# Optimization experiments

Measured on AMD Instinct MI355X. Metric: run time of the kernel, lower is better.

## Reference

```python
import jax, jax.numpy as jnp
import numpy as np

B, N, F, T, K, FO = 16, 1024, 64, 24, 3, 64


def setup_inputs() -> dict:
    key = jax.random.key(0)
    ks = jax.random.split(key, 8)
    sc = 0.05
    x = jax.random.normal(ks[0], (B, N, F, T), dtype=jnp.float32)
    W1 = jax.random.normal(ks[1], (T,), dtype=jnp.float32) * sc
    W2 = jax.random.normal(ks[2], (F, T), dtype=jnp.float32) * sc
    W3 = jax.random.normal(ks[3], (F,), dtype=jnp.float32) * sc
    bs = jax.random.normal(ks[4], (1, N, N), dtype=jnp.float32) * sc
    Vs = jax.random.normal(ks[5], (N, N), dtype=jnp.float32) * sc
    cheb = jax.random.normal(ks[6], (K, N, N), dtype=jnp.float32) * sc
    Theta = jax.random.normal(ks[7], (K, F, FO), dtype=jnp.float32) * sc
    return {"x": x, "W1": W1, "W2": W2, "W3": W3, "bs": bs, "Vs": Vs,
            "cheb": cheb, "Theta": Theta}


def spatial_attention(x, W1, W2, W3, bs, Vs):
    # x: (B,N,F,T) -> S: (B,N,N)
    lhs = jnp.einsum('bnft,t->bnf', x, W1)          # (B,N,F)
    lhs = jnp.einsum('bnf,ft->bnt', lhs, W2)        # (B,N,T)
    rhs = jnp.einsum('f,bnft->btn', W3, x)          # (B,T,N)
    product = jnp.einsum('bnt,btm->bnm', lhs, rhs)  # (B,N,N)
    S = jnp.einsum('ik,bkj->bij', Vs, jax.nn.sigmoid(product + bs))
    return jax.nn.softmax(S, axis=1)


def reference(x, W1, W2, W3, bs, Vs, cheb, Theta):
    # x: (B,N,F,T); cheb: (K,N,N); Theta: (K,F,FO)
    S = spatial_attention(x, W1, W2, W3, bs, Vs)    # (B,N,N)
    out = jnp.zeros((x.shape[0], x.shape[1], Theta.shape[2], x.shape[3]),
                    dtype=x.dtype)
    for k in range(cheb.shape[0]):                  # small fixed K
        Tat = cheb[k] * S                           # (B,N,N) attention-masked T_k
        # T_k_with_at.permute(0,2,1) @ graph_signal, vectorized over t
        r = jnp.einsum('bnm,bnft->bmft', Tat, x)    # (B,N,F,T)
        out = out + jnp.einsum('bmft,fo->bmot', r, Theta[k])
    return jax.nn.relu(out)                         # (B,N,FO,T)
```

## Files before the change

### kernel.cpp

```cpp
#include <hip/hip_runtime.h>
#include <math.h>

#define Bc 16
#define Nc 1024
#define Fc 64
#define Tc 24
#define Kc 3
#define FOc 64
#define Cc (Fc*Tc)
#define KKc (Kc*Nc)

typedef __attribute__((ext_vector_type(8))) short short8;
typedef __attribute__((ext_vector_type(8))) unsigned short u16x8;
typedef __attribute__((ext_vector_type(4))) float f32x4;

__device__ __forceinline__ unsigned short f2bf(float f) {
  unsigned u = __float_as_uint(f);
  u += 0x7fff + ((u >> 16) & 1);
  return (unsigned short)(u >> 16);
}
__device__ __forceinline__ float bf2f(unsigned short h) {
  return __uint_as_float((unsigned)h << 16);
}

#define GLL16(g, l) __builtin_amdgcn_global_load_lds( \
    (const __attribute__((address_space(1))) void*)(g), \
    (__attribute__((address_space(3))) void*)(l), 16, 0, 0)

__device__ __forceinline__ f32x4 mfma16(short8 a, short8 b, f32x4 c) {
  return __builtin_amdgcn_mfma_f32_16x16x32_bf16(a, b, c, 0, 0, 0);
}

__device__ __forceinline__ void gemm_core(
    const unsigned short* __restrict__ Ag, const unsigned short* __restrict__ Bg,
    int lda, int ldb, int K,
    unsigned short* As, unsigned short* Bs,
    int wave, int lane, f32x4 acc[4][4]) {
  int sr = lane >> 3;
  int sc = ((lane & 7) ^ sr) * 8;
  const unsigned short* a0 = Ag + (size_t)(wave * 32 + sr) * lda + sc;
  const unsigned short* b0 = Bg + (size_t)(wave * 32 + sr) * ldb + sc;
  unsigned short* asw = As + (wave * 32) * 64;
  unsigned short* bsw = Bs + (wave * 32) * 64;
  int rw = (wave >> 1) * 64, cw = (wave & 1) * 64;
  int frow = lane & 15;
  int q = lane >> 4;
  int p0 = (q ^ (frow & 7)) * 8;
  int p1 = ((q | 4) ^ (frow & 7)) * 8;
  for (int k0 = 0; k0 < K; k0 += 64) {
    #pragma unroll
    for (int c = 0; c < 4; ++c) {
      GLL16(a0 + (size_t)(c * 8) * lda + k0, asw + (c * 8) * 64);
      GLL16(b0 + (size_t)(c * 8) * ldb + k0, bsw + (c * 8) * 64);
    }
    __syncthreads();
    #pragma unroll
    for (int h = 0; h < 2; ++h) {
      int p = h ? p1 : p0;
      short8 afr[4], bfr[4];
      #pragma unroll
      for (int i = 0; i < 4; ++i)
        afr[i] = *(const short8*)&As[(rw + i * 16 + frow) * 64 + p];
      #pragma unroll
      for (int j = 0; j < 4; ++j)
        bfr[j] = *(const short8*)&Bs[(cw + j * 16 + frow) * 64 + p];
      #pragma unroll
      for (int i = 0; i < 4; ++i)
        #pragma unroll
        for (int j = 0; j < 4; ++j)
          acc[i][j] = mfma16(afr[i], bfr[j], acc[i][j]);
    }
    __syncthreads();
  }
}

__global__ __launch_bounds__(256) void xprep_kernel(
    const float* __restrict__ x, const float* __restrict__ W1,
    const float* __restrict__ W2, const float* __restrict__ W3,
    unsigned short* __restrict__ xt2, unsigned short* __restrict__ lhsb,
    unsigned short* __restrict__ rhsb) {
  __shared__ float ld[4 * 1560];
  __shared__ float af[4 * 64];
  int w = threadIdx.x >> 6, lane = threadIdx.x & 63;
  size_t n = (size_t)blockIdx.x * 4 + w;
  const float* xp = x + n * Cc;
  float* lw = ld + w * 1560;
  #pragma unroll
  for (int j = 0; j < 24; ++j) {
    int i = j * 64 + lane;
    int f = i / 24, t = i - f * 24;
    lw[t * 65 + f] = xp[i];
  }
  __syncthreads();
  float a = 0.f;
  #pragma unroll
  for (int t = 0; t < Tc; ++t) a += lw[t * 65 + lane] * W1[t];
  af[w * 64 + lane] = a;
  #pragma unroll
  for (int j = 0; j < 24; ++j)
    xt2[n * Cc + j * 64 + lane] = f2bf(lw[j * 65 + lane]);
  __syncthreads();
  float l = 0.f, r = 0.f;
  if (lane < Tc) {
    #pragma unroll 8
    for (int f = 0; f < Fc; ++f) {
      l += af[w * 64 + f] * W2[f * Tc + lane];
      r += W3[f] * lw[lane * 65 + f];
    }
  }
  lhsb[n * 64 + lane] = (lane < Tc) ? f2bf(l) : (unsigned short)0;
  rhsb[n * 64 + lane] = (lane < Tc) ? f2bf(r) : (unsigned short)0;
}

__global__ __launch_bounds__(256) void misc_kernel(
    const float* __restrict__ Vs, const float* __restrict__ Theta,
    const float* __restrict__ bs, unsigned short* __restrict__ Vsbf,
    unsigned short* __restrict__ tcat, float* __restrict__ bsT) {
  __shared__ float t[64 * 65];
  int bid = blockIdx.x, tid = threadIdx.x;
  if (bid < 1024) {
    int i = (bid * 256 + tid) * 4;
    float4 v = *(const float4*)&Vs[i];
    ushort4 o;
    o.x = f2bf(v.x); o.y = f2bf(v.y); o.z = f2bf(v.z); o.w = f2bf(v.w);
    *(ushort4*)&Vsbf[i] = o;
  } else if (bid < 1088) {
    int i = (bid - 1024) * 256 + tid;
    int m2 = i >> 6, f = i & 63;
    int k = m2 >> 6, o = m2 & 63;
    tcat[i] = (m2 < 192) ? f2bf(Theta[((size_t)k * Fc + f) * FOc + o])
                         : (unsigned short)0;
  } else {
    int id = bid - 1088;
    int p0 = (id >> 4) * 64, q0 = (id & 15) * 64;
    #pragma unroll
    for (int s = 0; s < 4; ++s) {
      int qr = (tid >> 4) + s * 16, pc = (tid & 15) * 4;
      float4 v = *(const float4*)&bs[(size_t)(q0 + qr) * Nc + p0 + pc];
      t[(pc + 0) * 65 + qr] = v.x;
      t[(pc + 1) * 65 + qr] = v.y;
      t[(pc + 2) * 65 + qr] = v.z;
      t[(pc + 3) * 65 + qr] = v.w;
    }
    __syncthreads();
    #pragma unroll
    for (int s = 0; s < 4; ++s) {
      int pr = (tid >> 4) + s * 16, qc = (tid & 15) * 4;
      float4 v = {t[pr * 65 + qc], t[pr * 65 + qc + 1],
                  t[pr * 65 + qc + 2], t[pr * 65 + qc + 3]};
      *(float4*)&bsT[(size_t)(p0 + pr) * Nc + q0 + qc] = v;
    }
  }
}

__global__ __launch_bounds__(256) void chebT_kernel(
    const float* __restrict__ cheb, float* __restrict__ chebT) {
  int k = blockIdx.z;
  int n0 = blockIdx.y * 64, m0 = blockIdx.x * 64;
  __shared__ float t[64 * 65];
  const float* src = cheb + (size_t)k * Nc * Nc;
  float* dst = chebT + (size_t)k * Nc * Nc;
  int tid = threadIdx.x;
  #pragma unroll
  for (int s = 0; s < 4; ++s) {
    int nr = (tid >> 4) + s * 16, mc = (tid & 15) * 4;
    float4 v = *(const float4*)&src[(size_t)(n0 + nr) * Nc + m0 + mc];
    t[(mc + 0) * 65 + nr] = v.x;
    t[(mc + 1) * 65 + nr] = v.y;
    t[(mc + 2) * 65 + nr] = v.z;
    t[(mc + 3) * 65 + nr] = v.w;
  }
  __syncthreads();
  #pragma unroll
  for (int s = 0; s < 4; ++s) {
    int mr = (tid >> 4) + s * 16, nc = (tid & 15) * 4;
    float4 v = {t[mr * 65 + nc], t[mr * 65 + nc + 1], t[mr * 65 + nc + 2], t[mr * 65 + nc + 3]};
    *(float4*)&dst[(size_t)(m0 + mr) * Nc + n0 + nc] = v;
  }
}

__global__ __launch_bounds__(256) void masksoft_kernel(
    const float* __restrict__ chebT, const unsigned short* __restrict__ ST,
    unsigned short* __restrict__ Acat, int bbase) {
  int m  = blockIdx.x & (Nc - 1);
  int bl = blockIdx.x >> 10;
  int tid = threadIdx.x;
  const unsigned short* sp = ST + ((size_t)(bbase + bl) * Nc + m) * Nc;
  ushort4 s4 = *(const ushort4*)(sp + tid * 4);
  float v0 = bf2f(s4.x), v1 = bf2f(s4.y), v2 = bf2f(s4.z), v3 = bf2f(s4.w);
  __shared__ float redm[4], reds[4];
  int wave = tid >> 6, lane = tid & 63;
  float mx = fmaxf(fmaxf(v0, v1), fmaxf(v2, v3));
  #pragma unroll
  for (int off = 32; off; off >>= 1) mx = fmaxf(mx, __shfl_xor(mx, off));
  if (lane == 0) redm[wave] = mx;
  __syncthreads();
  mx = fmaxf(fmaxf(redm[0], redm[1]), fmaxf(redm[2], redm[3]));
  float e0 = __expf(v0 - mx), e1 = __expf(v1 - mx);
  float e2 = __expf(v2 - mx), e3 = __expf(v3 - mx);
  float sm = e0 + e1 + e2 + e3;
  #pragma unroll
  for (int off = 32; off; off >>= 1) sm += __shfl_xor(sm, off);
  if (lane == 0) reds[wave] = sm;
  __syncthreads();
  float inv = 1.f / (reds[0] + reds[1] + reds[2] + reds[3]);
  e0 *= inv; e1 *= inv; e2 *= inv; e3 *= inv;
  unsigned short* ap = Acat + ((size_t)bl * Nc + m) * KKc + tid * 4;
  #pragma unroll
  for (int k = 0; k < Kc; ++k) {
    float4 c = *(const float4*)&chebT[((size_t)k * Nc + m) * Nc + tid * 4];
    ushort4 o;
    o.x = f2bf(c.x * e0); o.y = f2bf(c.y * e1);
    o.z = f2bf(c.z * e2); o.w = f2bf(c.w * e3);
    *(ushort4*)(ap + k * Nc) = o;
  }
}

template <int MODE>
__global__ __launch_bounds__(256) void mfma_gemm_bt(
    const unsigned short* __restrict__ A, const unsigned short* __restrict__ B,
    void* __restrict__ Cv, const float* __restrict__ bias, int K, int CN,
    long long Abatch, long long Bbatch, long long Cbatch) {
  __shared__ unsigned short As[128 * 64];
  __shared__ unsigned short Bs[128 * 64];
  int gx = gridDim.x, gy = gridDim.y;
  int nwg = gx * gy * gridDim.z;
  int bid = blockIdx.x + gx * (blockIdx.y + gy * blockIdx.z);
  int xcd = bid & 7, idx = bid >> 3;
  int qq = nwg >> 3, rr = nwg & 7;
  int lin = (xcd < rr ? xcd * (qq + 1) : rr * (qq + 1) + (xcd - rr) * qq) + idx;
  int b = lin / (gx * gy);
  int rem = lin - b * (gx * gy);
  int by = rem / gx, bx = rem - by * gx;
  int tid = threadIdx.x, wave = tid >> 6, lane = tid & 63;
  const unsigned short* Ag = A + (size_t)b * Abatch + (size_t)by * 128 * K;
  const unsigned short* Bg = B + (size_t)b * Bbatch + (size_t)bx * 128 * K;
  f32x4 zero = {0.f, 0.f, 0.f, 0.f};
  f32x4 acc[4][4];
  #pragma unroll
  for (int i = 0; i < 4; ++i)
    #pragma unroll
    for (int j = 0; j < 4; ++j) acc[i][j] = zero;
  gemm_core(Ag, Bg, K, K, K, As, Bs, wave, lane, acc);
  int rw = (wave >> 1) * 64, cw = (wave & 1) * 64;
  int q = lane >> 4, cl = lane & 15;
  #pragma unroll
  for (int i = 0; i < 4; ++i)
    #pragma unroll
    for (int e = 0; e < 4; ++e) {
      size_t P = (size_t)by * 128 + rw + i * 16 + q * 4 + e;
      #pragma unroll
      for (int j = 0; j < 4; ++j) {
        size_t Q = (size_t)bx * 128 + cw + j * 16 + cl;
        if (MODE == 0) {
          ((unsigned short*)Cv)[(size_t)b * Cbatch + P * CN + Q] = f2bf(acc[i][j][e]);
        } else if (MODE == 1) {
          ((float*)Cv)[(size_t)b * Cbatch + P * CN + Q] = fmaxf(acc[i][j][e], 0.f);
        } else {
          float v = acc[i][j][e] + bias[P * CN + Q];
          ((unsigned short*)Cv)[(size_t)b * Cbatch + P * CN + Q] =
              f2bf(1.f / (1.f + __expf(-v)));
        }
      }
    }
}

__global__ __launch_bounds__(256) void y2_gemm(
    const unsigned short* __restrict__ tcat, const unsigned short* __restrict__ xt2,
    unsigned short* __restrict__ ycat, int bbase) {
  __shared__ unsigned short As[128 * 64];
  __shared__ unsigned short Bs[128 * 64];
  int z = blockIdx.z;
  int bl = z / 24, t = z - bl * 24;
  int tid = threadIdx.x, wave = tid >> 6, lane = tid & 63;
  const unsigned short* Ag = tcat + (size_t)blockIdx.y * 128 * 64;
  const unsigned short* Bg = xt2 + ((size_t)(bbase + bl) * Nc + (size_t)blockIdx.x * 128) * Cc
                             + (size_t)t * 64;
  f32x4 zero = {0.f, 0.f, 0.f, 0.f};
  f32x4 acc[4][4];
  #pragma unroll
  for (int i = 0; i < 4; ++i)
    #pragma unroll
    for (int j = 0; j < 4; ++j) acc[i][j] = zero;
  gemm_core(Ag, Bg, 64, Cc, 64, As, Bs, wave, lane, acc);
  int rw = (wave >> 1) * 64, cw = (wave & 1) * 64;
  int q = lane >> 4, cl = lane & 15;
  unsigned short* yb = ycat + (size_t)bl * Cc * KKc + (size_t)t * KKc;
  #pragma unroll
  for (int i = 0; i < 4; ++i)
    #pragma unroll
    for (int e = 0; e < 4; ++e) {
      int m2 = blockIdx.y * 128 + rw + i * 16 + q * 4 + e;
      if (m2 < 192) {
        int kk = m2 >> 6, o = m2 & 63;
        unsigned short* dst = yb + (size_t)o * 24 * KKc + kk * Nc;
        #pragma unroll
        for (int j = 0; j < 4; ++j)
          dst[blockIdx.x * 128 + cw + j * 16 + cl] = f2bf(acc[i][j][e]);
      }
    }
}

extern "C" void kernel_launch(void* const* d_in, const int* in_sizes, int n_in,
                              void* d_out, int out_size, void* d_ws, size_t ws_size,
                              hipStream_t stream) {
  const float* x     = (const float*)d_in[0];
  const float* W1    = (const float*)d_in[1];
  const float* W2    = (const float*)d_in[2];
  const float* W3    = (const float*)d_in[3];
  const float* bs    = (const float*)d_in[4];
  const float* Vs    = (const float*)d_in[5];
  const float* cheb  = (const float*)d_in[6];
  const float* Theta = (const float*)d_in[7];
  float* out = (float*)d_out;

  int passes, blcount;
  if (ws_size >= 348160000ULL) { passes = 1; blcount = 16; }
  else                         { passes = 2; blcount = 8;  }

  char* w = (char*)d_ws;
  size_t Y  = (size_t)blcount * Cc * KKc * 2;
  size_t A2 = (size_t)blcount * Nc * KKc * 2;
  unsigned short* ycat = (unsigned short*)w;
  unsigned short* Acat = (unsigned short*)(w + Y);
  unsigned short* ST   = (unsigned short*)(w + Y + A2);
  float* chebT         = (float*)(w + Y + A2 + 33554432);
  unsigned short* xt2  = (unsigned short*)(w + Y + A2 + 46137344);
  unsigned short* tcat = (unsigned short*)(w + Y + A2 + 96468992);
  unsigned short* lhsb = (unsigned short*)w;
  unsigned short* rhsb = (unsigned short*)(w + 2097152);
  unsigned short* sigT = (unsigned short*)(w + 4194304);
  float* bsT           = (float*)(w + 37748736);
  unsigned short* Vsbf = (unsigned short*)(w + 41943040);

  xprep_kernel<<<Bc * Nc / 4, 256, 0, stream>>>(x, W1, W2, W3, xt2, lhsb, rhsb);
  misc_kernel<<<1344, 256, 0, stream>>>(Vs, Theta, bs, Vsbf, tcat, bsT);
  mfma_gemm_bt<2><<<dim3(8, 8, 16), 256, 0, stream>>>(
      rhsb, lhsb, sigT, bsT, 64, Nc,
      (long long)Nc * 64, (long long)Nc * 64, (long long)Nc * Nc);
  mfma_gemm_bt<0><<<dim3(8, 8, 16), 256, 0, stream>>>(
      sigT, Vsbf, ST, nullptr, Nc, Nc,
      (long long)Nc * Nc, 0LL, (long long)Nc * Nc);
  chebT_kernel<<<dim3(16, 16, 3), 256, 0, stream>>>(cheb, chebT);

  for (int pass = 0; pass < passes; ++pass) {
    int bbase = pass * blcount;
    masksoft_kernel<<<blcount * Nc, 256, 0, stream>>>(chebT, ST, Acat, bbase);
    y2_gemm<<<dim3(Nc / 128, 2, blcount * 24), 256, 0, stream>>>(tcat, xt2, ycat, bbase);
    mfma_gemm_bt<1><<<dim3(Cc / 128, Nc / 128, blcount), 256, 0, stream>>>(
        Acat, ycat, out + (size_t)bbase * Nc * Cc, nullptr, KKc, Cc,
        (long long)Nc * KKc, (long long)Cc * KKc, (long long)Nc * Cc);
  }
}
```

Before: 542.8 us.

## Add 256-row double-buffered GEMM with XCD-aware block remap for big GEMMs

Introduces a 512-thread GEMM kernel with 256xJN*64 output tiles, double-buffered LDS staging via global_load_lds, and a block-index remap that groups consecutive tiles per XCD. It replaces the 128x128 GEMM for the Vs@sigmoid product and for the final large Acat x ycat GEMM with ReLU epilogue. Larger tiles raise arithmetic intensity and overlap loads with MFMA work. The cost is much higher register and LDS use per block, which lowers occupancy, and a reduced grid for the smaller GEMM.

After: 577.1 us. 6.3% more time.

```diff
diff --git a/kernel.cpp b/kernel.cpp
--- a/kernel.cpp
+++ b/kernel.cpp
@@ -11,7 +11,6 @@
 #define KKc (Kc*Nc)
 
 typedef __attribute__((ext_vector_type(8))) short short8;
-typedef __attribute__((ext_vector_type(8))) unsigned short u16x8;
 typedef __attribute__((ext_vector_type(4))) float f32x4;
 
 __device__ __forceinline__ unsigned short f2bf(float f) {
@@ -72,6 +71,116 @@
     }
     __syncthreads();
   }
+}
+
+template <int MODE, int JN>
+__global__ __launch_bounds__(512) void gemm256(
+    const unsigned short* __restrict__ A, const unsigned short* __restrict__ B,
+    void* __restrict__ Cv, int K, int CN,
+    long long Abatch, long long Bbatch, long long Cbatch) {
+  __shared__ unsigned short S[2 * (256 + JN * 64) * 64];
+  const int BN  = JN * 64;
+  const int BUF = (256 + BN) * 64;
+
+  int gx = gridDim.x, gy = gridDim.y;
+  int nwg = gx * gy * gridDim.z;
+  int bid = blockIdx.x + gx * (blockIdx.y + gy * blockIdx.z);
+  int xcd = bid & 7, idx = bid >> 3;
+  int qq = nwg >> 3, rr = nwg & 7;
+  int lin = (xcd < rr ? xcd * (qq + 1) : rr * (qq + 1) + (xcd - rr) * qq) + idx;
+  int b = lin / (gx * gy);
+  int rem = lin - b * (gx * gy);
+  int by = rem / gx, bx = rem - by * gx;
+
+  int tid = threadIdx.x, wave = tid >> 6, lane = tid & 63;
+  const unsigned short* Ag = A + (size_t)b * Abatch + (size_t)by * 256 * K;
+  const unsigned short* Bg = B + (size_t)b * Bbatch + (size_t)bx * BN * K;
+
+  int sr = lane >> 3;
+  int sc = ((lane & 7) ^ sr) * 8;
+  const unsigned short* a0 = Ag + (size_t)(wave * 32 + sr) * K + sc;
+  const unsigned short* b0 = Bg + (size_t)(wave * 32 + sr) * K + sc;
+  unsigned short* asw0 = S + wave * 32 * 64;
+  unsigned short* bsw0 = S + 256 * 64 + wave * 32 * 64;
+  unsigned short* asw1 = asw0 + BUF;
+  unsigned short* bsw1 = bsw0 + BUF;
+
+  int wm = wave >> 2, wn = wave & 3;
+  int rw = wm * 128;
+  int cw = wn * (JN * 16);
+  int frow = lane & 15;
+  int q = lane >> 4;
+  int p0 = (q ^ (frow & 7)) * 8;
+  int p1 = ((q | 4) ^ (frow & 7)) * 8;
+
+  f32x4 zero = {0.f, 0.f, 0.f, 0.f};
+  f32x4 acc[8][JN];
+  #pragma unroll
+  for (int i = 0; i < 8; ++i)
+    #pragma unroll
+    for (int j = 0; j < JN; ++j) acc[i][j] = zero;
+
+  auto STAGE = [&](unsigned short* asw, unsigned short* bsw, int k0) {
+    #pragma unroll
+    for (int c = 0; c < 4; ++c)
+      GLL16(a0 + (size_t)(c * 8) * K + k0, asw + (c * 8) * 64);
+    if (wave < 2 * JN) {
+      #pragma unroll
+      for (int c = 0; c < 4; ++c)
+        GLL16(b0 + (size_t)(c * 8) * K + k0, bsw + (c * 8) * 64);
+    }
+  };
+  auto COMPUTE = [&](const unsigned short* As, const unsigned short* Bs) {
+    #pragma unroll
+    for (int h = 0; h < 2; ++h) {
+      int p = h ? p1 : p0;
+      short8 afr[8], bfr[JN];
+      #pragma unroll
+      for (int i = 0; i < 8; ++i)
+        afr[i] = *(const short8*)&As[(rw + i * 16 + frow) * 64 + p];
+      #pragma unroll
+      for (int j = 0; j < JN; ++j)
+        bfr[j] = *(const short8*)&Bs[(cw + j * 16 + frow) * 64 + p];
+      #pragma unroll
+      for (int i = 0; i < 8; ++i)
+        #pragma unroll
+        for (int j = 0; j < JN; ++j)
+          acc[i][j] = mfma16(afr[i], bfr[j], acc[i][j]);
+    }
+  };
+
+  STAGE(asw0, bsw0, 0);
+  __syncthreads();
+  int k0 = 0;
+  for (;;) {
+    if (k0 + 64 < K) STAGE(asw1, bsw1, k0 + 64);
+    COMPUTE(S, S + 256 * 64);
+    __syncthreads();
+    k0 += 64;
+    if (k0 >= K) break;
+    if (k0 + 64 < K) STAGE(asw0, bsw0, k0 + 64);
+    COMPUTE(S + BUF, S + BUF + 256 * 64);
+    __syncthreads();
+    k0 += 64;
+    if (k0 >= K) break;
+  }
+
+  int cl = lane & 15;
+  #pragma unroll
+  for (int i = 0; i < 8; ++i)
+    #pragma unroll
+    for (int e = 0; e < 4; ++e) {
+      size_t P = (size_t)by * 256 + rw + i * 16 + q * 4 + e;
+      #pragma unroll
+      for (int j = 0; j < JN; ++j) {
+        size_t Q = (size_t)bx * BN + cw + j * 16 + cl;
+        if (MODE == 0) {
+          ((unsigned short*)Cv)[(size_t)b * Cbatch + P * CN + Q] = f2bf(acc[i][j][e]);
+        } else {
+          ((float*)Cv)[(size_t)b * Cbatch + P * CN + Q] = fmaxf(acc[i][j][e], 0.f);
+        }
+      }
+    }
 }
 
 __global__ __launch_bounds__(256) void xprep_kernel(
@@ -338,8 +447,8 @@
   mfma_gemm_bt<2><<<dim3(8, 8, 16), 256, 0, stream>>>(
       rhsb, lhsb, sigT, bsT, 64, Nc,
       (long long)Nc * 64, (long long)Nc * 64, (long long)Nc * Nc);
-  mfma_gemm_bt<0><<<dim3(8, 8, 16), 256, 0, stream>>>(
-      sigT, Vsbf, ST, nullptr, Nc, Nc,
+  gemm256<0, 4><<<dim3(4, 4, 16), 512, 0, stream>>>(
+      sigT, Vsbf, ST, Nc, Nc,
       (long long)Nc * Nc, 0LL, (long long)Nc * Nc);
   chebT_kernel<<<dim3(16, 16, 3), 256, 0, stream>>>(cheb, chebT);
 
@@ -347,8 +456,8 @@
     int bbase = pass * blcount;
     masksoft_kernel<<<blcount * Nc, 256, 0, stream>>>(chebT, ST, Acat, bbase);
     y2_gemm<<<dim3(Nc / 128, 2, blcount * 24), 256, 0, stream>>>(tcat, xt2, ycat, bbase);
-    mfma_gemm_bt<1><<<dim3(Cc / 128, Nc / 128, blcount), 256, 0, stream>>>(
-        Acat, ycat, out + (size_t)bbase * Nc * Cc, nullptr, KKc, Cc,
+    gemm256<1, 3><<<dim3(Cc / 192, Nc / 256, blcount), 512, 0, stream>>>(
+        Acat, ycat, out + (size_t)bbase * Nc * Cc, KKc, Cc,
         (long long)Nc * KKc, (long long)Cc * KKc, (long long)Nc * Cc);
   }
 }
```
